# Kernel tuning notes

Measured on AMD Instinct MI355X. Metric: run time of the kernel, lower is better.

## Reference

```python
import jax, jax.numpy as jnp
import numpy as np

TOKENS, HIDDEN, N_EXPERTS = 16384, 2048, 64
JITTER_EPS = 0.01
Z_LOSS_COEFF = 0.001


def setup_inputs() -> dict:
    key = jax.random.key(0)
    k1, k2 = jax.random.split(key)
    x = jax.random.normal(k1, (TOKENS, HIDDEN), dtype=jnp.float32)
    w = jax.random.normal(k2, (N_EXPERTS, HIDDEN), dtype=jnp.float32) * 0.02  # router weight [E,H]
    return {"x": x, "w": w}


def _route_pass(scores_sel, scores, jitter_eps):
    # scores_sel: logits possibly with -inf at already-selected expert (top-2 pass)
    # scores:     original logits (used for abs/clamp factor, as in torch code)
    mx = jnp.max(scores_sel, axis=-1, keepdims=True)                      # [N,1]
    factor = jnp.maximum(jnp.abs(scores), mx)                             # scores.abs().clamp(min=mx)
    mask = jax.lax.stop_gradient((mx - scores) / factor > 2.0 * jitter_eps)
    masked_logits = jnp.where(mask, -jnp.inf, scores_sel)
    # eval path (training=False): selected_experts = argmax of (masked-for-selection) scores
    sel = jnp.argmax(scores_sel, axis=-1)[..., None]                      # [N,1] int
    gates = jax.nn.softmax(masked_logits, axis=-1)
    # mask_for_one: selected == argmax(gates) holds deterministically in eval -> 1.0
    mult = jnp.take_along_axis(gates, sel, axis=-1)                       # [N,1]
    return mult, sel


def reference(x, w):
    logits = x @ w.T                                                      # [N,E]
    # z-loss (identity on logits in forward; scalar returned for completeness)
    z_loss = Z_LOSS_COEFF * jnp.mean(jnp.square(jax.nn.logsumexp(logits, axis=-1)))
    original_gates = jax.nn.softmax(logits, axis=-1)
    # top-1 pass
    m1, s1 = _route_pass(logits, logits, JITTER_EPS)
    # top-2 pass: mask out the first selection
    e_idx = jnp.arange(logits.shape[-1])[None, :]
    scores2 = jnp.where(e_idx == s1, -jnp.inf, logits)
    m2, s2 = _route_pass(scores2, logits, JITTER_EPS)
    multiplier = jnp.concatenate([m1, m2], axis=-1)                       # [N,2]
    selected_experts = jnp.concatenate([s1, s2], axis=-1)                 # [N,2]
    return multiplier, original_gates, selected_experts, z_loss
```

## Files before the change

kernel.cpp:

```cpp
#include <hip/hip_runtime.h>
#include <math.h>

#define TOKENS 16384
#define HIDDEN 2048
#define NEXP   64
#define MT     16
#define NBLK   (TOKENS / MT)

#define GATES_OFF (TOKENS * 2)
#define SEL_OFF   (GATES_OFF + TOKENS * NEXP)
#define Z_OFF     (SEL_OFF + TOKENS * 2)

#define WIMG_BYTES (NEXP * HIDDEN * 2 * 2)

typedef __attribute__((ext_vector_type(8))) _Float16 f16x8;
typedef __attribute__((ext_vector_type(4))) float    f32x4;

__device__ float    g_zacc = 0.f;
__device__ unsigned g_cnt  = 0u;

__device__ __forceinline__ float wave_sum64(float v) {
    #pragma unroll
    for (int s = 1; s < 64; s <<= 1) v += __shfl_xor(v, s, 64);
    return v;
}

__global__ __launch_bounds__(256) void wconvert(
    const float* __restrict__ w, uint4* __restrict__ wimg)
{
    const int s = blockIdx.x * 256 + threadIdx.x;
    const int c    = s >> 10;
    const int r    = s & 1023;
    const int l    = r & 63;
    const int nt   = (r >> 6) & 1;
    const int kh   = (r >> 7) & 1;
    const int term = (r >> 8) & 1;
    const int eh   = (r >> 9) & 1;
    const int e = eh * 32 + nt * 16 + (l & 15);
    const int k = c * 64 + kh * 32 + (l >> 4) * 8;

    const float* src = w + (size_t)e * HIDDEN + k;
    union { _Float16 f[8]; uint4 u; } o;
    #pragma unroll
    for (int j = 0; j < 8; ++j) {
        const float v = src[j];
        const _Float16 h = (_Float16)v;
        o.f[j] = (term == 0) ? h : (_Float16)((v - (float)h) * 4096.f);
    }
    wimg[s] = o.u;
}

__device__ __forceinline__ void cvt_split(const float4 a, const float4 b,
                                          f16x8& hi, f16x8& lo) {
    union { _Float16 f[8]; f16x8 v; } H, L;
    #pragma unroll
    for (int j = 0; j < 4; ++j) {
        const float s0 = (&a.x)[j];
        const float s1 = (&b.x)[j];
        const _Float16 h0 = (_Float16)s0;
        const _Float16 h1 = (_Float16)s1;
        H.f[j]     = h0;
        H.f[j + 4] = h1;
        L.f[j]     = (_Float16)((s0 - (float)h0) * 4096.f);
        L.f[j + 4] = (_Float16)((s1 - (float)h1) * 4096.f);
    }
    hi = H.v; lo = L.v;
}

struct Stage {
    float4 a0, a1;
    f16x8  bh[4], bl[4];
};

__device__ __forceinline__ void load_stage(Stage& S, const float* ax0,
                                           const uint4* wB, int s) {
    S.a0 = *(const float4*)(ax0 + s * 32);
    S.a1 = *(const float4*)(ax0 + s * 32 + 4);
    const uint4* p = wB + (s >> 1) * 1024 + (s & 1) * 128;
    S.bh[0] = *(const f16x8*)(p);
    S.bh[1] = *(const f16x8*)(p + 64);
    S.bh[2] = *(const f16x8*)(p + 512);
    S.bh[3] = *(const f16x8*)(p + 576);
    S.bl[0] = *(const f16x8*)(p + 256);
    S.bl[1] = *(const f16x8*)(p + 320);
    S.bl[2] = *(const f16x8*)(p + 768);
    S.bl[3] = *(const f16x8*)(p + 832);
}

__device__ __forceinline__ void consume_stage(
    const Stage& S, f32x4 (&acc0)[4], f32x4 (&acc1)[4])
{
    f16x8 Ah, Al;
    cvt_split(S.a0, S.a1, Ah, Al);
    #pragma unroll
    for (int g = 0; g < 4; ++g) {
        acc0[g] = __builtin_amdgcn_mfma_f32_16x16x32_f16(Ah, S.bh[g], acc0[g], 0, 0, 0);
        acc1[g] = __builtin_amdgcn_mfma_f32_16x16x32_f16(Ah, S.bl[g], acc1[g], 0, 0, 0);
        acc1[g] = __builtin_amdgcn_mfma_f32_16x16x32_f16(Al, S.bh[g], acc1[g], 0, 0, 0);
    }
}

__global__ __launch_bounds__(256, 3) void router_main(
    const float* __restrict__ x, const uint4* __restrict__ wimg,
    float* __restrict__ out)
{
    __shared__ __align__(16) float lg[4][MT * 66];
    __shared__ float zred[4];

    const int tid  = threadIdx.x;
    const int wv   = __builtin_amdgcn_readfirstlane(tid >> 6);
    const int lane = tid & 63;
    const int t0   = blockIdx.x * MT;

    const float* ax0 = x + (size_t)(t0 + (lane & 15)) * HIDDEN
                         + wv * 512 + (lane >> 4) * 8;

    const uint4* wB = wimg + wv * 8192 + lane;

    f32x4 acc0[4], acc1[4];
    #pragma unroll
    for (int g = 0; g < 4; ++g) { acc0[g] = (f32x4)0.f; acc1[g] = (f32x4)0.f; }

    Stage SA, SB;
    load_stage(SA, ax0, wB, 0);
    load_stage(SB, ax0, wB, 1);

    #pragma unroll
    for (int s = 0; s < 16; s += 2) {
        consume_stage(SA, acc0, acc1);
        if (s + 2 < 16) load_stage(SA, ax0, wB, s + 2);
        consume_stage(SB, acc0, acc1);
        if (s + 3 < 16) load_stage(SB, ax0, wB, s + 3);
    }

    #pragma unroll
    for (int g = 0; g < 4; ++g)
        #pragma unroll
        for (int r = 0; r < 4; ++r) {
            const int tok = (lane >> 4) * 4 + r;
            const int e   = (g >> 1) * 32 + (g & 1) * 16 + (lane & 15);
            lg[wv][tok * 66 + e] = acc0[g][r] + acc1[g][r] * (1.f / 4096.f);
        }
    __syncthreads();

    float zsum = 0.f;
    for (int tt = 0; tt < 4; ++tt) {
        const int t = wv * 4 + tt;
        const int li = t * 66 + lane;
        const float v = lg[0][li] + lg[1][li] + lg[2][li] + lg[3][li];

        float bv = v; int bi = lane;
        #pragma unroll
        for (int s = 1; s < 64; s <<= 1) {
            const float ov = __shfl_xor(bv, s, 64);
            const int   oi = __shfl_xor(bi, s, 64);
            if (ov > bv || (ov == bv && oi < bi)) { bv = ov; bi = oi; }
        }
        const float max1 = bv; const int s1 = bi;

        const float e1 = expf(v - max1);
        const float sume = wave_sum64(e1);
        out[GATES_OFF + (size_t)(t0 + t) * NEXP + lane] = e1 / sume;
        const float lse = max1 + logf(sume);
        zsum += lse * lse;

        const bool mask1 = (max1 - v) > 0.02f * fmaxf(fabsf(v), max1);
        const float sum1 = wave_sum64(mask1 ? 0.f : e1);

        float bv2 = (lane == s1) ? -INFINITY : v; int bi2 = lane;
        #pragma unroll
        for (int s = 1; s < 64; s <<= 1) {
            const float ov = __shfl_xor(bv2, s, 64);
            const int   oi = __shfl_xor(bi2, s, 64);
            if (ov > bv2 || (ov == bv2 && oi < bi2)) { bv2 = ov; bi2 = oi; }
        }
        const float max2 = bv2; const int s2 = bi2;

        const bool mask2 = (max2 - v) > 0.02f * fmaxf(fabsf(v), max2);
        const float p2v = (mask2 || lane == s1) ? 0.f : expf(v - max2);
        const float sum2 = wave_sum64(p2v);

        if (lane == 0) {
            const size_t trow = (size_t)(t0 + t) * 2;
            out[trow + 0] = 1.f / sum1;
            out[trow + 1] = 1.f / sum2;
            out[SEL_OFF + trow + 0] = (float)s1;
            out[SEL_OFF + trow + 1] = (float)s2;
        }
    }

    if (lane == 0) zred[wv] = zsum;
    __syncthreads();

    if (tid == 0) {
        const float bz = zred[0] + zred[1] + zred[2] + zred[3];
        atomicAdd(&g_zacc, bz);
        __threadfence();
        const unsigned old = atomicAdd(&g_cnt, 1u);
        if (old == NBLK - 1) {
            __threadfence();
            const float tot = atomicExch(&g_zacc, 0.f);
            atomicExch(&g_cnt, 0u);
            out[Z_OFF] = 0.001f * (tot / (float)TOKENS);
        }
    }
}

extern "C" void kernel_launch(void* const* d_in, const int* in_sizes, int n_in,
                              void* d_out, int out_size, void* d_ws, size_t ws_size,
                              hipStream_t stream) {
    const float* x = (const float*)d_in[0];
    const float* w = (const float*)d_in[1];
    float* out = (float*)d_out;

    uint4* wimg = (uint4*)d_ws;

    wconvert<<<128, 256, 0, stream>>>(w, wimg);
    router_main<<<NBLK, 256, 0, stream>>>(x, wimg, out);
}
```

Baseline: 241.5 us.

## Replace atomic z-loss reduction with partials plus final kernel; pin MFMA schedule

Each block now writes its z-loss partial to workspace, and a small single-block kernel sums the partials. This replaces the global atomic counter and last-block-finishes pattern, removing the atomics and thread fences from the main kernel's tail. Scheduling barriers are added around each load/consume stage to keep the compiler from reordering loads and MFMAs across the software pipeline. The cost is an extra kernel launch and possibly worse instruction interleaving if the compiler's own schedule was better.

```diff
diff --git a/kernel.cpp b/kernel.cpp
--- a/kernel.cpp
+++ b/kernel.cpp
@@ -15,9 +15,6 @@
 
 typedef __attribute__((ext_vector_type(8))) _Float16 f16x8;
 typedef __attribute__((ext_vector_type(4))) float    f32x4;
-
-__device__ float    g_zacc = 0.f;
-__device__ unsigned g_cnt  = 0u;
 
 __device__ __forceinline__ float wave_sum64(float v) {
     #pragma unroll
@@ -102,7 +99,7 @@
 
 __global__ __launch_bounds__(256, 3) void router_main(
     const float* __restrict__ x, const uint4* __restrict__ wimg,
-    float* __restrict__ out)
+    float* __restrict__ out, float* __restrict__ zpartial)
 {
     __shared__ __align__(16) float lg[4][MT * 66];
     __shared__ float zred[4];
@@ -124,13 +121,17 @@
     Stage SA, SB;
     load_stage(SA, ax0, wB, 0);
     load_stage(SB, ax0, wB, 1);
+    __builtin_amdgcn_sched_barrier(0);
 
     #pragma unroll
     for (int s = 0; s < 16; s += 2) {
         consume_stage(SA, acc0, acc1);
         if (s + 2 < 16) load_stage(SA, ax0, wB, s + 2);
+        __builtin_amdgcn_sched_barrier(0);
+
         consume_stage(SB, acc0, acc1);
         if (s + 3 < 16) load_stage(SB, ax0, wB, s + 3);
+        __builtin_amdgcn_sched_barrier(0);
     }
 
     #pragma unroll
@@ -191,18 +192,23 @@
 
     if (lane == 0) zred[wv] = zsum;
     __syncthreads();
-
+    if (tid == 0)
+        zpartial[blockIdx.x] = zred[0] + zred[1] + zred[2] + zred[3];
+}
+
+__global__ __launch_bounds__(256) void zfinal(
+    const float* __restrict__ zpartial, float* __restrict__ out)
+{
+    const int tid = threadIdx.x;
+    float v = zpartial[tid] + zpartial[tid + 256]
+            + zpartial[tid + 512] + zpartial[tid + 768];
+    v = wave_sum64(v);
+    __shared__ float red[4];
+    if ((tid & 63) == 0) red[tid >> 6] = v;
+    __syncthreads();
     if (tid == 0) {
-        const float bz = zred[0] + zred[1] + zred[2] + zred[3];
-        atomicAdd(&g_zacc, bz);
-        __threadfence();
-        const unsigned old = atomicAdd(&g_cnt, 1u);
-        if (old == NBLK - 1) {
-            __threadfence();
-            const float tot = atomicExch(&g_zacc, 0.f);
-            atomicExch(&g_cnt, 0u);
-            out[Z_OFF] = 0.001f * (tot / (float)TOKENS);
-        }
+        const float tot = red[0] + red[1] + red[2] + red[3];
+        out[Z_OFF] = 0.001f * (tot / (float)TOKENS);
     }
 }
 
@@ -213,8 +219,10 @@
     const float* w = (const float*)d_in[1];
     float* out = (float*)d_out;
 
-    uint4* wimg = (uint4*)d_ws;
+    uint4* wimg     = (uint4*)d_ws;
+    float* zpartial = (float*)((char*)d_ws + WIMG_BYTES);
 
     wconvert<<<128, 256, 0, stream>>>(w, wimg);
-    router_main<<<NBLK, 256, 0, stream>>>(x, wimg, out);
-}
+    router_main<<<NBLK, 256, 0, stream>>>(x, wimg, out, zpartial);
+    zfinal<<<1, 256, 0, stream>>>(zpartial, out);
+}
```

Result: faster. 218.8 us (-9.4%).
